# Kernel tuning notes

Measured on AMD Instinct MI355X. Metric: run time of the kernel, lower is better.

Reference implementation:

```python
import jax, jax.numpy as jnp
import numpy as np

B, F, H, E, O = 512, 512, 512, 8, 512  # batch, feature, hidden, experts, out_frame


def setup_inputs() -> dict:
    key = jax.random.key(0)
    ks = jax.random.split(key, 14)
    u = lambda k, shape, s: jax.random.uniform(k, shape, jnp.float32) * s
    return {
        "x": jax.random.normal(ks[0], (B, F), jnp.float32),
        # gating MLP params (torch Linear: y = x @ W.T + b)
        "gw0": u(ks[1], (H, F), 0.04) - 0.02,
        "gb0": jnp.zeros((H,), jnp.float32),
        "gw1": u(ks[2], (H, H), 0.04) - 0.02,
        "gb1": jnp.zeros((H,), jnp.float32),
        "gw2": u(ks[3], (E, H), 0.04) - 0.02,
        "gb2": jnp.zeros((E,), jnp.float32),
        # expert weight/bias banks
        "alpha0": u(ks[4], (E, H, F), 0.01),
        "beta0": jnp.zeros((E, H, 1), jnp.float32),
        "alpha1": u(ks[5], (E, H, H), 0.01),
        "beta1": jnp.zeros((E, H, 1), jnp.float32),
        "alpha2": u(ks[6], (E, O, H), 0.01),
        "beta2": jnp.zeros((E, O, 1), jnp.float32),
    }


def reference(x, gw0, gb0, gw1, gb1, gw2, gb2,
              alpha0, beta0, alpha1, beta1, alpha2, beta2):
    # gating network
    h = jax.nn.elu(x @ gw0.T + gb0)
    h = jax.nn.elu(h @ gw1.T + gb1)
    g = jax.nn.softmax(h @ gw2.T + gb2, axis=1)  # [B, E]

    # per-sample blended weights (sum over experts of gate-scaled expert mats)
    blend_w = lambda a: jnp.einsum('be,ehf->bhf', g, a)
    blend_b = lambda b: jnp.einsum('be,eh->bh', g, b[..., 0])

    # per-sample 3-layer MLP (bmm with vector rhs == batched matvec)
    H1 = jax.nn.elu(jnp.einsum('bhf,bf->bh', blend_w(alpha0), x) + blend_b(beta0))
    H2 = jax.nn.elu(jnp.einsum('bhf,bf->bh', blend_w(alpha1), H1) + blend_b(beta1))
    H3 = jnp.einsum('bof,bf->bo', blend_w(alpha2), H2) + blend_b(beta2)
    return H3
```

## Files before the change

kernel.cpp:

```cpp
#include <hip/hip_runtime.h>
#include <hip/hip_bf16.h>
#include <math.h>

enum { Bq = 512, Fq = 512, Hq = 512, Eq = 8, Oq = 512 };

typedef __attribute__((ext_vector_type(8))) short short8;
typedef __attribute__((ext_vector_type(4))) float floatx4;

static __device__ __forceinline__ unsigned short f2bf(float f) {
  unsigned u = __float_as_uint(f);
  u += 0x7fffu + ((u >> 16) & 1u);
  return (unsigned short)(u >> 16);
}
static __device__ __forceinline__ float bf2f(unsigned short h) {
  return __uint_as_float(((unsigned)h) << 16);
}
static __device__ __forceinline__ float elu1(float v) {
  return v > 0.f ? v : (__expf(v) - 1.f);
}

typedef __attribute__((address_space(1))) const unsigned int gu32;
typedef __attribute__((address_space(3))) unsigned int lu32;
static __device__ __forceinline__ void gld16(const unsigned short* g,
                                             unsigned short* l) {
  __builtin_amdgcn_global_load_lds((gu32*)g, (lu32*)l, 16, 0, 0);
}

static __device__ __forceinline__ int swz(int q, int r) {
  return (q & ~7) | ((q ^ r) & 7);
}

__global__ __launch_bounds__(256) void cvt6_kernel(
    const float* __restrict__ b0, const float* __restrict__ b1,
    const float* __restrict__ b2, unsigned short* __restrict__ db0,
    unsigned short* __restrict__ db1, unsigned short* __restrict__ db2,
    const float* __restrict__ s0, const float* __restrict__ s1,
    const float* __restrict__ s2, unsigned short* __restrict__ ds0,
    unsigned short* __restrict__ ds1, unsigned short* __restrict__ ds2,
    int nb, int ns) {
  int i = blockIdx.x * 256 + threadIdx.x;
  const float4* s;
  unsigned short* d;
  int j;
  if (i < 3 * nb) {
    int seg = i / nb;
    j = i - seg * nb;
    s = (seg == 0) ? (const float4*)b0
      : (seg == 1) ? (const float4*)b1 : (const float4*)b2;
    d = (seg == 0) ? db0 : (seg == 1) ? db1 : db2;
  } else {
    int k = i - 3 * nb;
    if (k >= 3 * ns) return;
    int seg = k / ns;
    j = k - seg * ns;
    s = (seg == 0) ? (const float4*)s0
      : (seg == 1) ? (const float4*)s1 : (const float4*)s2;
    d = (seg == 0) ? ds0 : (seg == 1) ? ds1 : ds2;
  }
  float4 v = s[j];
  ushort4 o;
  o.x = f2bf(v.x); o.y = f2bf(v.y); o.z = f2bf(v.z); o.w = f2bf(v.w);
  *(ushort4*)(d + 4 * (size_t)j) = o;
}

__global__ __launch_bounds__(256) void gating_gemm(
    const unsigned short* __restrict__ A, const unsigned short* __restrict__ W,
    const float* __restrict__ bias, unsigned short* __restrict__ C) {
  __shared__ unsigned short As[32 * 512];
  __shared__ unsigned short Ws[32 * 512];
  const int tid = threadIdx.x;
  const int wave = tid >> 6, lane = tid & 63;
  const int wm = wave >> 1, wn = wave & 1;
  const int lr = lane & 15, lk = lane >> 4;
  const int m0 = blockIdx.y * 32, n0 = blockIdx.x * 32;
#pragma unroll
  for (int i = 0; i < 8; i++) {
    int c = tid + i * 256;
    int r = c >> 6, ql = c & 63;
    int qg = swz(ql, r);
    gld16(&A[(size_t)(m0 + r) * 512 + qg * 8], &As[(c & ~63) * 8]);
  }
#pragma unroll
  for (int i = 0; i < 8; i++) {
    int c = tid + i * 256;
    int r = c >> 6, ql = c & 63;
    int qg = swz(ql, r);
    gld16(&W[(size_t)(n0 + r) * 512 + qg * 8], &Ws[(c & ~63) * 8]);
  }
  __syncthreads();
  const int rA = wm * 16 + lr, rB = wn * 16 + lr;
  floatx4 ac[4];
#pragma unroll
  for (int j = 0; j < 4; j++) ac[j] = (floatx4){0.f, 0.f, 0.f, 0.f};
#pragma unroll
  for (int t = 0; t < 4; t++) {
#pragma unroll
    for (int j = 0; j < 4; j++) {
      int q = ((j * 128 + t * 32) >> 3) + lk;
      short8 av = *(const short8*)&As[rA * 512 + swz(q, rA) * 8];
      short8 bv = *(const short8*)&Ws[rB * 512 + swz(q, rB) * 8];
      ac[j] = __builtin_amdgcn_mfma_f32_16x16x32_bf16(av, bv, ac[j], 0, 0, 0);
    }
  }
  floatx4 acc = (ac[0] + ac[1]) + (ac[2] + ac[3]);
  int n = n0 + wn * 16 + lr;
  float bn = bias[n];
#pragma unroll
  for (int r = 0; r < 4; r++) {
    int m = m0 + wm * 16 + lk * 4 + r;
    C[(size_t)m * 512 + n] = f2bf(elu1(acc[r] + bn));
  }
}

__global__ __launch_bounds__(256) void expert_gemm(
    const unsigned short* __restrict__ A,
    const unsigned short* __restrict__ Wb,
    const float* __restrict__ g,
    float* __restrict__ P) {
  __shared__ unsigned short As[64 * 256];
  __shared__ unsigned short Ws[64 * 256];
  const int tid = threadIdx.x;
  const int wave = tid >> 6, lane = tid & 63;
  const int wm = wave >> 1, wn = wave & 1;
  const int lr = lane & 15, lk = lane >> 4;
  const int nt = blockIdx.x;
  const int m0 = blockIdx.y * 64;
  const int ks = blockIdx.z;
  const int e = nt >> 3;
  const int n0g = nt * 64;
  const int n0l = (nt & 7) * 64;
  const int kbeg = ks * 256;
#pragma unroll
  for (int i = 0; i < 8; i++) {
    int c = tid + i * 256;
    int r = c >> 5, ql = c & 31;
    int qg = swz(ql, r);
    gld16(&A[(size_t)(m0 + r) * 512 + kbeg + qg * 8], &As[(c & ~63) * 8]);
  }
#pragma unroll
  for (int i = 0; i < 8; i++) {
    int c = tid + i * 256;
    int r = c >> 5, ql = c & 31;
    int qg = swz(ql, r);
    gld16(&Wb[(size_t)(n0g + r) * 512 + kbeg + qg * 8], &Ws[(c & ~63) * 8]);
  }
  __syncthreads();
  floatx4 acc[2][2];
#pragma unroll
  for (int i = 0; i < 2; i++)
#pragma unroll
    for (int j = 0; j < 2; j++) acc[i][j] = (floatx4){0.f, 0.f, 0.f, 0.f};
  const int rA0 = wm * 32 + lr, rB0 = wn * 32 + lr;
#pragma unroll
  for (int kk = 0; kk < 256; kk += 32) {
    int q = (kk >> 3) + lk;
    short8 af[2], bf[2];
#pragma unroll
    for (int i = 0; i < 2; i++) {
      int r = rA0 + i * 16;
      af[i] = *(const short8*)&As[r * 256 + swz(q, r) * 8];
    }
#pragma unroll
    for (int j = 0; j < 2; j++) {
      int r = rB0 + j * 16;
      bf[j] = *(const short8*)&Ws[r * 256 + swz(q, r) * 8];
    }
#pragma unroll
    for (int i = 0; i < 2; i++)
#pragma unroll
      for (int j = 0; j < 2; j++)
        acc[i][j] = __builtin_amdgcn_mfma_f32_16x16x32_bf16(af[i], bf[j],
                                                            acc[i][j], 0, 0, 0);
  }
  float* Po = P + (size_t)(ks * 8 + e) * Bq * Hq;
#pragma unroll
  for (int i = 0; i < 2; i++) {
#pragma unroll
    for (int j = 0; j < 2; j++) {
#pragma unroll
      for (int r = 0; r < 4; r++) {
        int m = m0 + wm * 32 + i * 16 + lk * 4 + r;
        int n = n0l + wn * 32 + j * 16 + lr;
        Po[(size_t)m * 512 + n] = acc[i][j][r] * g[m * Eq + e];
      }
    }
  }
}

__global__ __launch_bounds__(64) void gate_kernel(
    const unsigned short* __restrict__ G1,
    const float* __restrict__ gw2,
    const float* __restrict__ gb2,
    float* __restrict__ g) {
  int b = blockIdx.x;
  int lane = threadIdx.x;
  float xv[8];
#pragma unroll
  for (int t = 0; t < 8; t++) xv[t] = bf2f(G1[(size_t)b * Hq + t * 64 + lane]);
  float le[Eq];
#pragma unroll
  for (int e = 0; e < Eq; e++) {
    float p = 0.f;
#pragma unroll
    for (int t = 0; t < 8; t++)
      p += xv[t] * gw2[(size_t)e * Hq + t * 64 + lane];
#pragma unroll
    for (int o = 32; o > 0; o >>= 1) p += __shfl_xor(p, o);
    le[e] = p + gb2[e];
  }
  float m = le[0];
#pragma unroll
  for (int e = 1; e < Eq; e++) m = fmaxf(m, le[e]);
  float s = 0.f;
#pragma unroll
  for (int e = 0; e < Eq; e++) {
    le[e] = __expf(le[e] - m);
    s += le[e];
  }
  float inv = 1.f / s;
  if (lane == 0) {
#pragma unroll
    for (int e = 0; e < Eq; e++) g[(size_t)b * Eq + e] = le[e] * inv;
  }
}

template <int ACT>
__global__ __launch_bounds__(256) void reduce_kernel(
    const float* __restrict__ P,
    const float* __restrict__ g,
    const float* __restrict__ beta,
    unsigned short* __restrict__ outb, float* __restrict__ outf) {
  int idx = blockIdx.x * 256 + threadIdx.x;
  int b = idx >> 7, h4 = (idx & 127) << 2;
  float4 s = {0.f, 0.f, 0.f, 0.f};
#pragma unroll
  for (int z = 0; z < 16; z++) {
    float4 v = *(const float4*)&P[((size_t)z * Bq + b) * Hq + h4];
    s.x += v.x; s.y += v.y; s.z += v.z; s.w += v.w;
  }
  const float* gb = g + (size_t)b * Eq;
#pragma unroll
  for (int e = 0; e < Eq; e++) {
    float ge = gb[e];
    float4 bv = *(const float4*)&beta[e * Hq + h4];
    s.x += ge * bv.x; s.y += ge * bv.y; s.z += ge * bv.z; s.w += ge * bv.w;
  }
  if (ACT) {
    ushort4 o;
    o.x = f2bf(elu1(s.x)); o.y = f2bf(elu1(s.y));
    o.z = f2bf(elu1(s.z)); o.w = f2bf(elu1(s.w));
    *(ushort4*)&outb[(size_t)idx * 4] = o;
  } else {
    *(float4*)&outf[(size_t)idx * 4] = s;
  }
}

extern "C" void kernel_launch(void* const* d_in, const int* in_sizes, int n_in,
                              void* d_out, int out_size, void* d_ws,
                              size_t ws_size, hipStream_t stream) {
  const float* x = (const float*)d_in[0];
  const float* gw0 = (const float*)d_in[1];
  const float* gb0 = (const float*)d_in[2];
  const float* gw1 = (const float*)d_in[3];
  const float* gb1 = (const float*)d_in[4];
  const float* gw2 = (const float*)d_in[5];
  const float* gb2 = (const float*)d_in[6];
  const float* alpha0 = (const float*)d_in[7];
  const float* beta0 = (const float*)d_in[8];
  const float* alpha1 = (const float*)d_in[9];
  const float* beta1 = (const float*)d_in[10];
  const float* alpha2 = (const float*)d_in[11];
  const float* beta2 = (const float*)d_in[12];
  float* out = (float*)d_out;

  char* ws = (char*)d_ws;
  auto alloc = [&](size_t bytes) {
    char* p = ws;
    ws += (bytes + 255) & ~(size_t)255;
    return p;
  };
  unsigned short* xb = (unsigned short*)alloc((size_t)Bq * Fq * 2);
  unsigned short* gw0b = (unsigned short*)alloc((size_t)Hq * Fq * 2);
  unsigned short* gw1b = (unsigned short*)alloc((size_t)Hq * Hq * 2);
  unsigned short* a0b = (unsigned short*)alloc((size_t)Eq * Hq * Fq * 2);
  unsigned short* a1b = (unsigned short*)alloc((size_t)Eq * Hq * Hq * 2);
  unsigned short* a2b = (unsigned short*)alloc((size_t)Eq * Oq * Hq * 2);
  unsigned short* G0b = (unsigned short*)alloc((size_t)Bq * Hq * 2);
  unsigned short* G1b = (unsigned short*)alloc((size_t)Bq * Hq * 2);
  unsigned short* H1b = (unsigned short*)alloc((size_t)Bq * Hq * 2);
  unsigned short* H2b = (unsigned short*)alloc((size_t)Bq * Hq * 2);
  float* gates = (float*)alloc((size_t)Bq * Eq * 4);
  float* P = (float*)alloc((size_t)16 * Bq * Hq * 4);

  {
    int nb = (Eq * Hq * Fq) / 4, ns = (Bq * Fq) / 4;
    int total = 3 * nb + 3 * ns;
    cvt6_kernel<<<(total + 255) / 256, 256, 0, stream>>>(
        alpha0, alpha1, alpha2, a0b, a1b, a2b, x, gw0, gw1, xb, gw0b, gw1b,
        nb, ns);
  }

  dim3 gg(16, 16);
  gating_gemm<<<gg, 256, 0, stream>>>(xb, gw0b, gb0, G0b);
  gating_gemm<<<gg, 256, 0, stream>>>(G0b, gw1b, gb1, G1b);

  gate_kernel<<<Bq, 64, 0, stream>>>(G1b, gw2, gb2, gates);

  dim3 ge(64, 8, 2);
  dim3 gr((Bq * Hq / 4) / 256);
  expert_gemm<<<ge, 256, 0, stream>>>(xb, a0b, gates, P);
  reduce_kernel<1><<<gr, 256, 0, stream>>>(P, gates, beta0, H1b, nullptr);
  expert_gemm<<<ge, 256, 0, stream>>>(H1b, a1b, gates, P);
  reduce_kernel<1><<<gr, 256, 0, stream>>>(P, gates, beta1, H2b, nullptr);
  expert_gemm<<<ge, 256, 0, stream>>>(H2b, a2b, gates, P);
  reduce_kernel<0><<<gr, 256, 0, stream>>>(P, gates, beta2, nullptr, out);
}
```

Measured before the change: 149.5 us.

## Fuse expert gate-weighted sum into expert GEMM with double-buffered weight tiles

The expert GEMM now loops over all 8 experts inside one block, keeping the activation tile resident and double-buffering each expert's weight tile in shared memory. It applies the gate weights in registers and writes a single partial per K-split instead of 16 per-expert partial planes. This removes most of the partial-sum traffic to global memory and the 16-way read in the reduce kernel. In exchange, tiles shrink to 32x32, giving lower MFMA reuse per load, and there is a barrier per expert step.

```diff
diff --git a/kernel.cpp b/kernel.cpp
--- a/kernel.cpp
+++ b/kernel.cpp
@@ -77,15 +77,13 @@
   for (int i = 0; i < 8; i++) {
     int c = tid + i * 256;
     int r = c >> 6, ql = c & 63;
-    int qg = swz(ql, r);
-    gld16(&A[(size_t)(m0 + r) * 512 + qg * 8], &As[(c & ~63) * 8]);
+    gld16(&A[(size_t)(m0 + r) * 512 + swz(ql, r) * 8], &As[(c & ~63) * 8]);
   }
 #pragma unroll
   for (int i = 0; i < 8; i++) {
     int c = tid + i * 256;
     int r = c >> 6, ql = c & 63;
-    int qg = swz(ql, r);
-    gld16(&W[(size_t)(n0 + r) * 512 + qg * 8], &Ws[(c & ~63) * 8]);
+    gld16(&W[(size_t)(n0 + r) * 512 + swz(ql, r) * 8], &Ws[(c & ~63) * 8]);
   }
   __syncthreads();
   const int rA = wm * 16 + lr, rB = wn * 16 + lr;
@@ -117,73 +115,77 @@
     const unsigned short* __restrict__ Wb,
     const float* __restrict__ g,
     float* __restrict__ P) {
-  __shared__ unsigned short As[64 * 256];
-  __shared__ unsigned short Ws[64 * 256];
+  __shared__ unsigned short As[32 * 256];
+  __shared__ unsigned short Ws[2][32 * 256];
   const int tid = threadIdx.x;
   const int wave = tid >> 6, lane = tid & 63;
   const int wm = wave >> 1, wn = wave & 1;
   const int lr = lane & 15, lk = lane >> 4;
-  const int nt = blockIdx.x;
-  const int m0 = blockIdx.y * 64;
-  const int ks = blockIdx.z;
-  const int e = nt >> 3;
-  const int n0g = nt * 64;
-  const int n0l = (nt & 7) * 64;
-  const int kbeg = ks * 256;
-#pragma unroll
-  for (int i = 0; i < 8; i++) {
+  const int m0 = blockIdx.y * 32, n0 = blockIdx.x * 32;
+  const int kz = blockIdx.z, kbeg = kz * 256;
+
+#pragma unroll
+  for (int i = 0; i < 4; i++) {
     int c = tid + i * 256;
     int r = c >> 5, ql = c & 31;
-    int qg = swz(ql, r);
-    gld16(&A[(size_t)(m0 + r) * 512 + kbeg + qg * 8], &As[(c & ~63) * 8]);
-  }
-#pragma unroll
-  for (int i = 0; i < 8; i++) {
+    gld16(&A[(size_t)(m0 + r) * 512 + kbeg + swz(ql, r) * 8],
+          &As[(c & ~63) * 8]);
+  }
+#pragma unroll
+  for (int i = 0; i < 4; i++) {
     int c = tid + i * 256;
     int r = c >> 5, ql = c & 31;
-    int qg = swz(ql, r);
-    gld16(&Wb[(size_t)(n0g + r) * 512 + kbeg + qg * 8], &Ws[(c & ~63) * 8]);
-  }
-  __syncthreads();
-  floatx4 acc[2][2];
-#pragma unroll
-  for (int i = 0; i < 2; i++)
-#pragma unroll
-    for (int j = 0; j < 2; j++) acc[i][j] = (floatx4){0.f, 0.f, 0.f, 0.f};
-  const int rA0 = wm * 32 + lr, rB0 = wn * 32 + lr;
-#pragma unroll
-  for (int kk = 0; kk < 256; kk += 32) {
-    int q = (kk >> 3) + lk;
-    short8 af[2], bf[2];
-#pragma unroll
-    for (int i = 0; i < 2; i++) {
-      int r = rA0 + i * 16;
-      af[i] = *(const short8*)&As[r * 256 + swz(q, r) * 8];
-    }
-#pragma unroll
-    for (int j = 0; j < 2; j++) {
-      int r = rB0 + j * 16;
-      bf[j] = *(const short8*)&Ws[r * 256 + swz(q, r) * 8];
-    }
-#pragma unroll
-    for (int i = 0; i < 2; i++)
-#pragma unroll
-      for (int j = 0; j < 2; j++)
-        acc[i][j] = __builtin_amdgcn_mfma_f32_16x16x32_bf16(af[i], bf[j],
-                                                            acc[i][j], 0, 0, 0);
-  }
-  float* Po = P + (size_t)(ks * 8 + e) * Bq * Hq;
-#pragma unroll
-  for (int i = 0; i < 2; i++) {
-#pragma unroll
-    for (int j = 0; j < 2; j++) {
-#pragma unroll
-      for (int r = 0; r < 4; r++) {
-        int m = m0 + wm * 32 + i * 16 + lk * 4 + r;
-        int n = n0l + wn * 32 + j * 16 + lr;
-        Po[(size_t)m * 512 + n] = acc[i][j][r] * g[m * Eq + e];
+    gld16(&Wb[(size_t)(n0 + r) * 512 + kbeg + swz(ql, r) * 8],
+          &Ws[0][(c & ~63) * 8]);
+  }
+  float g8[4][8];
+#pragma unroll
+  for (int r = 0; r < 4; r++) {
+    int m = m0 + wm * 16 + lk * 4 + r;
+    float4 ga = *(const float4*)&g[(size_t)m * 8];
+    float4 gb = *(const float4*)&g[(size_t)m * 8 + 4];
+    g8[r][0] = ga.x; g8[r][1] = ga.y; g8[r][2] = ga.z; g8[r][3] = ga.w;
+    g8[r][4] = gb.x; g8[r][5] = gb.y; g8[r][6] = gb.z; g8[r][7] = gb.w;
+  }
+
+  const int rA = wm * 16 + lr, rB = wn * 16 + lr;
+  floatx4 fin = {0.f, 0.f, 0.f, 0.f};
+#pragma unroll
+  for (int e = 0; e < 8; e++) {
+    __syncthreads();
+    if (e < 7) {
+      const unsigned short* Wn = Wb + ((size_t)(e + 1) * 512 + n0) * 512 + kbeg;
+#pragma unroll
+      for (int i = 0; i < 4; i++) {
+        int c = tid + i * 256;
+        int r = c >> 5, ql = c & 31;
+        gld16(&Wn[(size_t)r * 512 + swz(ql, r) * 8],
+              &Ws[(e + 1) & 1][(c & ~63) * 8]);
       }
     }
+    const unsigned short* wb = Ws[e & 1];
+    floatx4 c0 = {0.f, 0.f, 0.f, 0.f}, c1 = {0.f, 0.f, 0.f, 0.f};
+#pragma unroll
+    for (int s = 0; s < 8; s++) {
+      int q = s * 4 + lk;
+      short8 av = *(const short8*)&As[rA * 256 + swz(q, rA) * 8];
+      short8 bv = *(const short8*)&wb[rB * 256 + swz(q, rB) * 8];
+      if (s & 1)
+        c1 = __builtin_amdgcn_mfma_f32_16x16x32_bf16(av, bv, c1, 0, 0, 0);
+      else
+        c0 = __builtin_amdgcn_mfma_f32_16x16x32_bf16(av, bv, c0, 0, 0, 0);
+    }
+    floatx4 ae = c0 + c1;
+#pragma unroll
+    for (int r = 0; r < 4; r++) fin[r] += g8[r][e] * ae[r];
+  }
+
+  float* Po = P + (size_t)kz * Bq * Hq;
+  int n = n0 + wn * 16 + lr;
+#pragma unroll
+  for (int r = 0; r < 4; r++) {
+    int m = m0 + wm * 16 + lk * 4 + r;
+    Po[(size_t)m * 512 + n] = fin[r];
   }
 }
 
@@ -232,12 +234,9 @@
     unsigned short* __restrict__ outb, float* __restrict__ outf) {
   int idx = blockIdx.x * 256 + threadIdx.x;
   int b = idx >> 7, h4 = (idx & 127) << 2;
-  float4 s = {0.f, 0.f, 0.f, 0.f};
-#pragma unroll
-  for (int z = 0; z < 16; z++) {
-    float4 v = *(const float4*)&P[((size_t)z * Bq + b) * Hq + h4];
-    s.x += v.x; s.y += v.y; s.z += v.z; s.w += v.w;
-  }
+  float4 v0 = *(const float4*)&P[((size_t)b) * Hq + h4];
+  float4 v1 = *(const float4*)&P[((size_t)Bq + b) * Hq + h4];
+  float4 s = {v0.x + v1.x, v0.y + v1.y, v0.z + v1.z, v0.w + v1.w};
   const float* gb = g + (size_t)b * Eq;
 #pragma unroll
   for (int e = 0; e < Eq; e++) {
@@ -290,7 +289,7 @@
   unsigned short* H1b = (unsigned short*)alloc((size_t)Bq * Hq * 2);
   unsigned short* H2b = (unsigned short*)alloc((size_t)Bq * Hq * 2);
   float* gates = (float*)alloc((size_t)Bq * Eq * 4);
-  float* P = (float*)alloc((size_t)16 * Bq * Hq * 4);
+  float* P = (float*)alloc((size_t)2 * Bq * Hq * 4);
 
   {
     int nb = (Eq * Hq * Fq) / 4, ns = (Bq * Fq) / 4;
@@ -306,7 +305,7 @@
 
   gate_kernel<<<Bq, 64, 0, stream>>>(G1b, gw2, gb2, gates);
 
-  dim3 ge(64, 8, 2);
+  dim3 ge(16, 16, 2);
   dim3 gr((Bq * Hq / 4) / 256);
   expert_gemm<<<ge, 256, 0, stream>>>(xb, a0b, gates, P);
   reduce_kernel<1><<<gr, 256, 0, stream>>>(P, gates, beta0, H1b, nullptr);
```

Result: faster. 139.7 us (-6.6%).
